# Kernel tuning notes

Measured on AMD Instinct MI355X. Metric: run time of the kernel, lower is better.

## Reference

```python
import jax, jax.numpy as jnp
import numpy as np

N = 50000      # nodes
E = 800000     # edges (avg degree 16)
F_IN = 64      # node_features (== GENConv out, so no input projection)
H = 64         # hidden
EXP = 2 * H    # GENConv MLP expansion dim = 128
D2 = F_IN + H  # dense-block concat dim = SAGEConv in = 128
EPS_MSG = 1e-7 # GENConv message eps
BN_EPS = 1e-5


def setup_inputs() -> dict:
    key = jax.random.key(0)
    ks = jax.random.split(key, 16)
    g = lambda k, shape, fan: jax.random.normal(k, shape, jnp.float32) / np.sqrt(fan)
    return {
        "x": jax.random.normal(ks[0], (N, F_IN), jnp.float32),
        "edge_index": jax.random.randint(ks[1], (2, E), 0, N, jnp.int32),
        # GENConv MLP: Linear(64,128) -> BatchNorm(128) -> ReLU -> Linear(128,64)
        "W1": g(ks[2], (H, EXP), H), "b1": jnp.zeros((EXP,), jnp.float32),
        "gamma": jnp.ones((EXP,), jnp.float32), "beta": jnp.zeros((EXP,), jnp.float32),
        "W2": g(ks[3], (EXP, H), EXP), "b2": jnp.zeros((H,), jnp.float32),
        # SAGEConv project Linear(128,128), lin_l Linear(128,64), lin_r Linear(128,64,bias=False)
        "Wp": g(ks[4], (D2, D2), D2), "bp": jnp.zeros((D2,), jnp.float32),
        "Wl": g(ks[5], (D2, H), D2), "bl": jnp.zeros((H,), jnp.float32),
        "Wr": g(ks[6], (D2, H), D2),
        # fc Linear(64,1)
        "Wf": g(ks[7], (H, 1), H), "bf": jnp.zeros((1,), jnp.float32),
    }


def _forward(x, W1, b1, gamma, beta, W2, b2, Wp, bp, Wl, bl, Wr, Wf, bf, src, dst):
    n = x.shape[0]
    # ---- GENConv(aggr='softmax', t=1.0): msg = relu(x_j) + eps -------------
    msg = jax.nn.relu(x[src]) + EPS_MSG                       # [E, H]
    mmax = jax.ops.segment_max(msg, dst, num_segments=n)      # per-dst, per-feature max
    mmax = jax.lax.stop_gradient(jnp.where(jnp.isfinite(mmax), mmax, 0.0))
    e = jnp.exp(msg - mmax[dst])                              # t = 1.0
    denom = jax.ops.segment_sum(e, dst, num_segments=n)
    numer = jax.ops.segment_sum(e * msg, dst, num_segments=n)
    agg = numer / jnp.where(denom > 0, denom, 1.0)            # softmax aggregation
    out = agg + x                                             # residual with x_dst
    # GENConv MLP (BatchNorm in training mode: batch stats, biased var)
    h = out @ W1 + b1
    mu = h.mean(axis=0)
    var = h.var(axis=0)
    h = (h - mu) * jax.lax.rsqrt(var + BN_EPS) * gamma + beta
    h = jax.nn.relu(h) @ W2 + b2                              # [N, H]
    # ---- DeepGCNLayer block='dense': concat input ---------------------------
    x2 = jnp.concatenate([x, h], axis=-1)                     # [N, F_IN+H]
    x2 = jax.nn.sigmoid(x2)                                   # self.relu = Sigmoid()
    # ---- SAGEConv(project=True, aggr=DeepSetsAggregation()==sum) -----------
    xp = jax.nn.relu(x2 @ Wp + bp)                            # projected source feats
    aggr = jax.ops.segment_sum(xp[src], dst, num_segments=n)  # DeepSets w/o nns = sum
    out2 = aggr @ Wl + bl + x2 @ Wr                           # root uses UNprojected x2
    out2 = jax.nn.sigmoid(out2)
    logits = out2 @ Wf + bf                                   # [N, 1]
    probs = jax.nn.sigmoid(logits)                            # training branch
    return probs, logits


def reference(x, edge_index, W1, b1, gamma, beta, W2, b2, Wp, bp, Wl, bl, Wr, Wf, bf):
    src, dst = edge_index[0], edge_index[1]
    return _forward(x, W1, b1, gamma, beta, W2, b2, Wp, bp, Wl, bl, Wr, Wf, bf, src, dst)
```

## Files before the change

kernel.cpp:

```cpp
#include <hip/hip_runtime.h>

#define F_IN 64
#define HID 64
#define EXPD 128
#define D2 128
#define MAXDEG 64
#define NB 782
#define NBINB 98
#define SUBCAP 40
#define EPT 32

typedef __attribute__((ext_vector_type(8))) short bf16x8;
typedef __attribute__((ext_vector_type(4))) float f32x4;

__device__ __forceinline__ float sigmoidf_(float x) {
    return 1.0f / (1.0f + __expf(-x));
}
__device__ __forceinline__ unsigned bf16rne_(float f) {
    unsigned u = __float_as_uint(f);
    return (u + 0x7FFFu + ((u >> 16) & 1u)) >> 16;
}
__device__ __forceinline__ float bf16tof_(unsigned u16) {
    return __uint_as_float(u16 << 16);
}

__global__ __launch_bounds__(256) void k_bin(const int* __restrict__ ei,
                                             int* __restrict__ cnt2,
                                             unsigned* __restrict__ binned2,
                                             const float* __restrict__ x,
                                             unsigned short* __restrict__ x16,
                                             const float* __restrict__ W1,
                                             const float* __restrict__ W2,
                                             const float* __restrict__ Wp,
                                             const float* __restrict__ Wl,
                                             const float* __restrict__ Wr,
                                             short* __restrict__ dst,
                                             float* __restrict__ bnsums,
                                             int nE, int n, int nbinb) {
    int b = blockIdx.x;
    int tid = threadIdx.x;
    if (b < nbinb) {
        __shared__ int hist[NB];
        if (b == 0) bnsums[tid] = 0.f;
        for (int i = tid; i < NB; i += 256) hist[i] = 0;
        __syncthreads();
        unsigned ed[EPT];
        unsigned short rk[EPT];
        int e0 = b * (256 * EPT);
#pragma unroll
        for (int j = 0; j < EPT; ++j) {
            int e = e0 + j * 256 + tid;
            if (e < nE) {
                unsigned s = (unsigned)ei[e];
                unsigned d = (unsigned)ei[nE + e];
                ed[j] = s | (d << 16);
                rk[j] = (unsigned short)atomicAdd(&hist[d >> 6], 1);
            }
        }
        __syncthreads();
        for (int i = tid; i < NB; i += 256) cnt2[b * NB + i] = hist[i];
#pragma unroll
        for (int j = 0; j < EPT; ++j) {
            int e = e0 + j * 256 + tid;
            if (e < nE) {
                int bin = (ed[j] >> 16) >> 6;
                int r = (int)rk[j];
                if (r < SUBCAP)
                    binned2[((size_t)bin * nbinb + b) * SUBCAP + r] = ed[j];
            }
        }
        return;
    }
    b -= nbinb;
    if (b < 192) {
        int e = b * 256 + tid;
        const float* src;
        int K, N, base2;
        if (e < 8192)       { src = W1; K = 64;  N = 128; base2 = 0; }
        else if (e < 16384) { src = W2; K = 128; N = 64;  base2 = 8192; }
        else if (e < 32768) { src = Wp; K = 128; N = 128; base2 = 16384; }
        else if (e < 40960) { src = Wl; K = 128; N = 64;  base2 = 32768; }
        else                { src = Wr; K = 128; N = 64;  base2 = 40960; }
        int le = e - base2;
        int j = le & 7;
        int lane = (le >> 3) & 63;
        int n16 = lane & 15, q = lane >> 4;
        int rest = le >> 9;
        int KC = K / 32;
        int kc = rest % KC, nt = rest / KC;
        int k = kc * 32 + q * 8 + j;
        int col = nt * 16 + n16;
        dst[e] = (short)bf16rne_(src[(size_t)k * N + col]);
        return;
    }
    int i0 = (b - 192) * 1024 + tid * 4;
    if (i0 < n * F_IN) {
        float4 v = *(const float4*)(x + i0);
        uint2 pk;
        pk.x = bf16rne_(v.x) | (bf16rne_(v.y) << 16);
        pk.y = bf16rne_(v.z) | (bf16rne_(v.w) << 16);
        *(uint2*)(x16 + i0) = pk;
    }
}

__global__ __launch_bounds__(1024) void k_geng(const int* __restrict__ cnt2,
                                               const unsigned* __restrict__ binned2,
                                               const unsigned short* __restrict__ x16,
                                               const short* __restrict__ Wf,
                                               const float* __restrict__ b1,
                                               unsigned short* __restrict__ h16,
                                               float* __restrict__ bnsums,
                                               int* __restrict__ counts,
                                               unsigned short* __restrict__ csr,
                                               int n, int nbinb) {
    __shared__ unsigned short lcsr[64 * MAXDEG];
    __shared__ int lcnt[64];
    __shared__ int scnt[NBINB];
    __shared__ short As[64 * 64];
    __shared__ float bnred[256];
    const unsigned* x32 = (const unsigned*)x16;
    int tid = threadIdx.x;
    int w = tid >> 6;
    int lane = tid & 63;
    int H = lane >> 5, f2 = lane & 31;
    int b = blockIdx.x;
    int rblk = b * 64;
    if (tid < 64) lcnt[tid] = 0;
    if (tid < 256) bnred[tid] = 0.f;
    for (int i = tid; i < nbinb; i += 1024) {
        int c = cnt2[i * NB + b];
        scnt[i] = c < SUBCAP ? c : SUBCAP;
    }
    __syncthreads();
    const unsigned* esrc = binned2 + (size_t)b * nbinb * SUBCAP;
    int tot = nbinb * SUBCAP;
    for (int i = tid; i < tot; i += 1024) {
        int blk = i / SUBCAP;
        int r = i - blk * SUBCAP;
        if (r < scnt[blk]) {
            unsigned u = esrc[i];
            int dl = (int)(u >> 16) - rblk;
            int slot = atomicAdd(&lcnt[dl], 1);
            if (slot < MAXDEG) lcsr[dl * MAXDEG + slot] = (unsigned short)(u & 0xFFFF);
        }
    }
    __syncthreads();
    if (tid < 64 && rblk + tid < n) counts[rblk + tid] = lcnt[tid];
    {
        int nrows = n - rblk;
        nrows = nrows < 64 ? nrows : 64;
        int nu4 = nrows * 8;
        uint4* dstrow = (uint4*)(csr + (size_t)rblk * MAXDEG);
        for (int i = tid; i < nu4; i += 1024) dstrow[i] = ((const uint4*)lcsr)[i];
    }
    for (int t = 0; t < 4; ++t) {
        int rr = w * 4 + t;
        int v = rblk + rr;
        int q8 = f2 >> 2;
        int slot = ((rr >> 4) * 2 + (q8 >> 2)) * 64 + (q8 & 3) * 16 + (rr & 15);
        if (v < n) {
            int deg = lcnt[rr];
            deg = deg > MAXDEG ? MAXDEG : deg;
            int idx = 0;
            if (lane < deg) idx = (int)lcsr[rr * MAXDEG + lane];
            float d0 = 0.f, d1 = 0.f, n0 = 0.f, n1 = 0.f;
            int i = 0;
            for (; i + 16 <= deg; i += 16) {
                unsigned us[8];
#pragma unroll
                for (int tt = 0; tt < 8; ++tt) {
                    int s = __shfl(idx, i + tt * 2 + H, 64);
                    us[tt] = x32[(size_t)s * 32 + f2];
                }
#pragma unroll
                for (int tt = 0; tt < 8; ++tt) {
                    unsigned u = us[tt];
                    float m0 = fmaxf(bf16tof_(u & 0xFFFF), 0.f) + 1e-7f;
                    float m1 = fmaxf(bf16tof_(u >> 16), 0.f) + 1e-7f;
                    float e0 = __expf(m0), e1 = __expf(m1);
                    d0 += e0; d1 += e1;
                    n0 = fmaf(e0, m0, n0);
                    n1 = fmaf(e1, m1, n1);
                }
            }
            for (; i + 8 <= deg; i += 8) {
                int sA = __shfl(idx, i + 0 + H, 64);
                int sB = __shfl(idx, i + 2 + H, 64);
                int sC = __shfl(idx, i + 4 + H, 64);
                int sD = __shfl(idx, i + 6 + H, 64);
                unsigned uA = x32[(size_t)sA * 32 + f2];
                unsigned uB = x32[(size_t)sB * 32 + f2];
                unsigned uC = x32[(size_t)sC * 32 + f2];
                unsigned uD = x32[(size_t)sD * 32 + f2];
#pragma unroll
                for (int tt = 0; tt < 4; ++tt) {
                    unsigned u = tt == 0 ? uA : tt == 1 ? uB : tt == 2 ? uC : uD;
                    float m0 = fmaxf(bf16tof_(u & 0xFFFF), 0.f) + 1e-7f;
                    float m1 = fmaxf(bf16tof_(u >> 16), 0.f) + 1e-7f;
                    float e0 = __expf(m0), e1 = __expf(m1);
                    d0 += e0; d1 += e1;
                    n0 = fmaf(e0, m0, n0);
                    n1 = fmaf(e1, m1, n1);
                }
            }
            for (; i + 2 <= deg; i += 2) {
                int s = __shfl(idx, i + H, 64);
                unsigned u = x32[(size_t)s * 32 + f2];
                float m0 = fmaxf(bf16tof_(u & 0xFFFF), 0.f) + 1e-7f;
                float m1 = fmaxf(bf16tof_(u >> 16), 0.f) + 1e-7f;
                float e0 = __expf(m0), e1 = __expf(m1);
                d0 += e0; d1 += e1;
                n0 = fmaf(e0, m0, n0);
                n1 = fmaf(e1, m1, n1);
            }
            if (i < deg) {
                int s = __shfl(idx, i, 64);
                if (H == 0) {
                    unsigned u = x32[(size_t)s * 32 + f2];
                    float m0 = fmaxf(bf16tof_(u & 0xFFFF), 0.f) + 1e-7f;
                    float m1 = fmaxf(bf16tof_(u >> 16), 0.f) + 1e-7f;
                    float e0 = __expf(m0), e1 = __expf(m1);
                    d0 += e0; d1 += e1;
                    n0 = fmaf(e0, m0, n0);
                    n1 = fmaf(e1, m1, n1);
                }
            }
            d0 += __shfl_xor(d0, 32, 64);
            d1 += __shfl_xor(d1, 32, 64);
            n0 += __shfl_xor(n0, 32, 64);
            n1 += __shfl_xor(n1, 32, 64);
            if (H == 0) {
                float a0 = (deg > 0) ? (n0 / d0) : 0.f;
                float a1 = (deg > 0) ? (n1 / d1) : 0.f;
                unsigned xv = x32[(size_t)v * 32 + f2];
                float r0 = a0 + bf16tof_(xv & 0xFFFF);
                float r1 = a1 + bf16tof_(xv >> 16);
                *(unsigned*)(As + slot * 8 + (f2 & 3) * 2) =
                    bf16rne_(r0) | (bf16rne_(r1) << 16);
            }
        } else {
            if (H == 0) *(unsigned*)(As + slot * 8 + (f2 & 3) * 2) = 0u;
        }
    }
    __syncthreads();
    int L = lane;
    int q = L >> 4, n16 = L & 15;
    int mt = w & 3;
    int nt_base = (w >> 2) * 2;
    f32x4 acc[2];
#pragma unroll
    for (int nt = 0; nt < 2; ++nt) acc[nt] = (f32x4){0.f, 0.f, 0.f, 0.f};
#pragma unroll
    for (int kc = 0; kc < 2; ++kc) {
        bf16x8 a = *(const bf16x8*)(As + ((mt * 2 + kc) * 64 + L) * 8);
#pragma unroll
        for (int nt = 0; nt < 2; ++nt) {
            bf16x8 b2 = *(const bf16x8*)(Wf + (size_t)(((nt_base + nt) * 2 + kc) * 64 + L) * 8);
            acc[nt] = __builtin_amdgcn_mfma_f32_16x16x32_bf16(a, b2, acc[nt], 0, 0, 0);
        }
    }
#pragma unroll
    for (int nt = 0; nt < 2; ++nt) {
        int col = (nt_base + nt) * 16 + n16;
        float bv = b1[col];
        float s = 0.f, s2 = 0.f;
#pragma unroll
        for (int r = 0; r < 4; ++r) {
            int row = rblk + mt * 16 + q * 4 + r;
            float hv = acc[nt][r] + bv;
            if (row < n) {
                h16[(size_t)row * EXPD + col] = (unsigned short)bf16rne_(hv);
                s += hv;
                s2 = fmaf(hv, hv, s2);
            }
        }
        s += __shfl_xor(s, 16, 64);
        s += __shfl_xor(s, 32, 64);
        s2 += __shfl_xor(s2, 16, 64);
        s2 += __shfl_xor(s2, 32, 64);
        if (q == 0) {
            atomicAdd(&bnred[col], s);
            atomicAdd(&bnred[128 + col], s2);
        }
    }
    __syncthreads();
    if (tid < 256) atomicAdd(&bnsums[tid], bnred[tid]);
}

__global__ __launch_bounds__(256) void k_mlp2ab(const unsigned short* __restrict__ h16,
                                                const float* __restrict__ bnsums,
                                                const float* __restrict__ gamma,
                                                const float* __restrict__ beta,
                                                const short* __restrict__ Wf2,
                                                const float* __restrict__ b2,
                                                const unsigned short* __restrict__ x16,
                                                const short* __restrict__ Wfp,
                                                const short* __restrict__ Wfl,
                                                const short* __restrict__ Wfr,
                                                const float* __restrict__ bp,
                                                unsigned short* __restrict__ yp16,
                                                unsigned short* __restrict__ yr16,
                                                float inv_n, int n) {
    __shared__ short Bs[64 * 128];
    __shared__ short As[64 * 128];
    __shared__ float ssl[256];
    int tid = threadIdx.x;
    int rblk = blockIdx.x * 64;
    if (tid < 128) {
        float mu = bnsums[tid] * inv_n;
        float var = fmaf(-mu, mu, bnsums[128 + tid] * inv_n);
        float rs = rsqrtf(fmaxf(var, 0.f) + 1e-5f);
        float scale = gamma[tid] * rs;
        ssl[tid] = scale;
        ssl[128 + tid] = fmaf(-mu, scale, beta[tid]);
    }
    __syncthreads();
#pragma unroll
    for (int it = 0; it < 4; ++it) {
        int c = it * 256 + tid;
        int rr = c & 63, q8 = c >> 6;
        int gr = rblk + rr;
        gr = gr < n ? gr : n - 1;
        uint4 v = *(const uint4*)(h16 + (size_t)gr * EXPD + q8 * 8);
        float4 sc1 = *(const float4*)(ssl + q8 * 8);
        float4 sc2 = *(const float4*)(ssl + q8 * 8 + 4);
        float4 sh1 = *(const float4*)(ssl + 128 + q8 * 8);
        float4 sh2 = *(const float4*)(ssl + 128 + q8 * 8 + 4);
        float o0 = fmaxf(fmaf(bf16tof_(v.x & 0xFFFF), sc1.x, sh1.x), 0.f);
        float o1 = fmaxf(fmaf(bf16tof_(v.x >> 16),    sc1.y, sh1.y), 0.f);
        float o2 = fmaxf(fmaf(bf16tof_(v.y & 0xFFFF), sc1.z, sh1.z), 0.f);
        float o3 = fmaxf(fmaf(bf16tof_(v.y >> 16),    sc1.w, sh1.w), 0.f);
        float o4 = fmaxf(fmaf(bf16tof_(v.z & 0xFFFF), sc2.x, sh2.x), 0.f);
        float o5 = fmaxf(fmaf(bf16tof_(v.z >> 16),    sc2.y, sh2.y), 0.f);
        float o6 = fmaxf(fmaf(bf16tof_(v.w & 0xFFFF), sc2.z, sh2.z), 0.f);
        float o7 = fmaxf(fmaf(bf16tof_(v.w >> 16),    sc2.w, sh2.w), 0.f);
        uint4 pk;
        pk.x = bf16rne_(o0) | (bf16rne_(o1) << 16);
        pk.y = bf16rne_(o2) | (bf16rne_(o3) << 16);
        pk.z = bf16rne_(o4) | (bf16rne_(o5) << 16);
        pk.w = bf16rne_(o6) | (bf16rne_(o7) << 16);
        int slot = ((rr >> 4) * 4 + (q8 >> 2)) * 64 + (q8 & 3) * 16 + (rr & 15);
        *(uint4*)(Bs + slot * 8) = pk;
    }
#pragma unroll
    for (int it = 0; it < 2; ++it) {
        int c = it * 256 + tid;
        int rr = c & 63, q8 = c >> 6;
        int gr = rblk + rr;
        gr = gr < n ? gr : n - 1;
        uint4 v = *(const uint4*)(x16 + (size_t)gr * F_IN + q8 * 8);
        float o0 = sigmoidf_(bf16tof_(v.x & 0xFFFF));
        float o1 = sigmoidf_(bf16tof_(v.x >> 16));
        float o2 = sigmoidf_(bf16tof_(v.y & 0xFFFF));
        float o3 = sigmoidf_(bf16tof_(v.y >> 16));
        float o4 = sigmoidf_(bf16tof_(v.z & 0xFFFF));
        float o5 = sigmoidf_(bf16tof_(v.z >> 16));
        float o6 = sigmoidf_(bf16tof_(v.w & 0xFFFF));
        float o7 = sigmoidf_(bf16tof_(v.w >> 16));
        uint4 pk;
        pk.x = bf16rne_(o0) | (bf16rne_(o1) << 16);
        pk.y = bf16rne_(o2) | (bf16rne_(o3) << 16);
        pk.z = bf16rne_(o4) | (bf16rne_(o5) << 16);
        pk.w = bf16rne_(o6) | (bf16rne_(o7) << 16);
        int slot = ((rr >> 4) * 4 + (q8 >> 2)) * 64 + (q8 & 3) * 16 + (rr & 15);
        *(uint4*)(As + slot * 8) = pk;
    }
    __syncthreads();
    int L = tid & 63, w = tid >> 6;
    int q = L >> 4, n16 = L & 15;
    {
        int mtb = (w & 1) * 2, ntb = (w >> 1) * 2;
        f32x4 acch[2][2];
#pragma unroll
        for (int mt = 0; mt < 2; ++mt)
#pragma unroll
            for (int nt = 0; nt < 2; ++nt) acch[mt][nt] = (f32x4){0.f, 0.f, 0.f, 0.f};
#pragma unroll
        for (int kc = 0; kc < 4; ++kc) {
            bf16x8 a0 = *(const bf16x8*)(Bs + (((mtb + 0) * 4 + kc) * 64 + L) * 8);
            bf16x8 a1 = *(const bf16x8*)(Bs + (((mtb + 1) * 4 + kc) * 64 + L) * 8);
#pragma unroll
            for (int nt = 0; nt < 2; ++nt) {
                bf16x8 b = *(const bf16x8*)(Wf2 + (size_t)(((ntb + nt) * 4 + kc) * 64 + L) * 8);
                acch[0][nt] = __builtin_amdgcn_mfma_f32_16x16x32_bf16(a0, b, acch[0][nt], 0, 0, 0);
                acch[1][nt] = __builtin_amdgcn_mfma_f32_16x16x32_bf16(a1, b, acch[1][nt], 0, 0, 0);
            }
        }
#pragma unroll
        for (int nt = 0; nt < 2; ++nt) {
            int col = (ntb + nt) * 16 + n16;
            float bv = b2[col];
            int q8b = 8 + (col >> 3), jb = col & 7;
#pragma unroll
            for (int mt = 0; mt < 2; ++mt)
#pragma unroll
                for (int r = 0; r < 4; ++r) {
                    int rr2 = (w & 1) * 32 + mt * 16 + q * 4 + r;
                    float hv = sigmoidf_(acch[mt][nt][r] + bv);
                    int slot = ((rr2 >> 4) * 4 + (q8b >> 2)) * 64 + (q8b & 3) * 16 + (rr2 & 15);
                    As[slot * 8 + jb] = (short)bf16rne_(hv);
                }
        }
    }
    __syncthreads();
    int mt_base = (w & 1) * 2;
    int nt_base = (w >> 1) * 4;
    f32x4 acc[2][4];
    f32x4 accr[2][2];
#pragma unroll
    for (int mt = 0; mt < 2; ++mt) {
#pragma unroll
        for (int nt = 0; nt < 4; ++nt) acc[mt][nt] = (f32x4){0.f, 0.f, 0.f, 0.f};
#pragma unroll
        for (int nt = 0; nt < 2; ++nt) accr[mt][nt] = (f32x4){0.f, 0.f, 0.f, 0.f};
    }
#pragma unroll
    for (int kc = 0; kc < 4; ++kc) {
        bf16x8 a0 = *(const bf16x8*)(As + (((mt_base + 0) * 4 + kc) * 64 + L) * 8);
        bf16x8 a1 = *(const bf16x8*)(As + (((mt_base + 1) * 4 + kc) * 64 + L) * 8);
#pragma unroll
        for (int nt = 0; nt < 4; ++nt) {
            bf16x8 b = *(const bf16x8*)(Wfp + (size_t)(((nt_base + nt) * 4 + kc) * 64 + L) * 8);
            acc[0][nt] = __builtin_amdgcn_mfma_f32_16x16x32_bf16(a0, b, acc[0][nt], 0, 0, 0);
            acc[1][nt] = __builtin_amdgcn_mfma_f32_16x16x32_bf16(a1, b, acc[1][nt], 0, 0, 0);
        }
#pragma unroll
        for (int nt = 0; nt < 2; ++nt) {
            bf16x8 b = *(const bf16x8*)(Wfr + (size_t)((((w >> 1) * 2 + nt) * 4 + kc) * 64 + L) * 8);
            accr[0][nt] = __builtin_amdgcn_mfma_f32_16x16x32_bf16(a0, b, accr[0][nt], 0, 0, 0);
            accr[1][nt] = __builtin_amdgcn_mfma_f32_16x16x32_bf16(a1, b, accr[1][nt], 0, 0, 0);
        }
    }
#pragma unroll
    for (int nt = 0; nt < 2; ++nt) {
        int col = ((w >> 1) * 2 + nt) * 16 + n16;
#pragma unroll
        for (int mt = 0; mt < 2; ++mt)
#pragma unroll
            for (int r = 0; r < 4; ++r) {
                int row = rblk + (w & 1) * 32 + mt * 16 + q * 4 + r;
                if (row < n)
                    yr16[(size_t)row * HID + col] = (unsigned short)bf16rne_(accr[mt][nt][r]);
            }
    }
#pragma unroll
    for (int nt = 0; nt < 4; ++nt) {
        int kk = (nt_base + nt) * 16 + n16;
        float bv = bp[kk];
        int q8b = kk >> 3, jb = kk & 7;
#pragma unroll
        for (int mt = 0; mt < 2; ++mt)
#pragma unroll
            for (int r = 0; r < 4; ++r) {
                int rr2 = (w & 1) * 32 + mt * 16 + q * 4 + r;
                float xv = fmaxf(acc[mt][nt][r] + bv, 0.f);
                int slot = ((rr2 >> 4) * 4 + (q8b >> 2)) * 64 + (q8b & 3) * 16 + (rr2 & 15);
                Bs[slot * 8 + jb] = (short)bf16rne_(xv);
            }
    }
    __syncthreads();
    f32x4 acc2[4];
#pragma unroll
    for (int nt = 0; nt < 4; ++nt) acc2[nt] = (f32x4){0.f, 0.f, 0.f, 0.f};
#pragma unroll
    for (int kc = 0; kc < 4; ++kc) {
        bf16x8 a = *(const bf16x8*)(Bs + ((w * 4 + kc) * 64 + L) * 8);
#pragma unroll
        for (int nt = 0; nt < 4; ++nt) {
            bf16x8 b = *(const bf16x8*)(Wfl + (size_t)((nt * 4 + kc) * 64 + L) * 8);
            acc2[nt] = __builtin_amdgcn_mfma_f32_16x16x32_bf16(a, b, acc2[nt], 0, 0, 0);
        }
    }
#pragma unroll
    for (int nt = 0; nt < 4; ++nt) {
        int col = nt * 16 + n16;
#pragma unroll
        for (int r = 0; r < 4; ++r) {
            int row = rblk + w * 16 + q * 4 + r;
            if (row < n)
                yp16[(size_t)row * HID + col] = (unsigned short)bf16rne_(acc2[nt][r]);
        }
    }
}

__global__ __launch_bounds__(256) void k_sagef(const unsigned short* __restrict__ yp16,
                                               const int* __restrict__ counts,
                                               const unsigned short* __restrict__ csr,
                                               const unsigned short* __restrict__ yr16,
                                               const float* __restrict__ bl,
                                               const float* __restrict__ Wfv,
                                               const float* __restrict__ bf,
                                               float* __restrict__ out, int n) {
    const unsigned* yp32 = (const unsigned*)yp16;
    int wid = threadIdx.x >> 6;
    int lane = threadIdx.x & 63;
    int H = lane >> 5, f2 = lane & 31;
    int v = blockIdx.x * 4 + wid;
    if (v >= n) return;
    int deg = counts[v];
    deg = deg > MAXDEG ? MAXDEG : deg;
    int idx = 0;
    if (lane < deg) idx = (int)csr[(size_t)v * MAXDEG + lane];
    float a0 = 0.f, a1 = 0.f;
    int i = 0;
    for (; i + 16 <= deg; i += 16) {
        unsigned us[8];
#pragma unroll
        for (int tt = 0; tt < 8; ++tt) {
            int s = __shfl(idx, i + tt * 2 + H, 64);
            us[tt] = yp32[(size_t)s * 32 + f2];
        }
#pragma unroll
        for (int tt = 0; tt < 8; ++tt) {
            a0 += bf16tof_(us[tt] & 0xFFFF);
            a1 += bf16tof_(us[tt] >> 16);
        }
    }
    for (; i + 8 <= deg; i += 8) {
        int sA = __shfl(idx, i + 0 + H, 64);
        int sB = __shfl(idx, i + 2 + H, 64);
        int sC = __shfl(idx, i + 4 + H, 64);
        int sD = __shfl(idx, i + 6 + H, 64);
        unsigned uA = yp32[(size_t)sA * 32 + f2];
        unsigned uB = yp32[(size_t)sB * 32 + f2];
        unsigned uC = yp32[(size_t)sC * 32 + f2];
        unsigned uD = yp32[(size_t)sD * 32 + f2];
        a0 += bf16tof_(uA & 0xFFFF) + bf16tof_(uB & 0xFFFF) +
              bf16tof_(uC & 0xFFFF) + bf16tof_(uD & 0xFFFF);
        a1 += bf16tof_(uA >> 16) + bf16tof_(uB >> 16) +
              bf16tof_(uC >> 16) + bf16tof_(uD >> 16);
    }
    for (; i + 2 <= deg; i += 2) {
        int s = __shfl(idx, i + H, 64);
        unsigned u = yp32[(size_t)s * 32 + f2];
        a0 += bf16tof_(u & 0xFFFF);
        a1 += bf16tof_(u >> 16);
    }
    if (i < deg) {
        int s = __shfl(idx, i, 64);
        if (H == 0) {
            unsigned u = yp32[(size_t)s * 32 + f2];
            a0 += bf16tof_(u & 0xFFFF);
            a1 += bf16tof_(u >> 16);
        }
    }
    a0 += __shfl_xor(a0, 32, 64);
    a1 += __shfl_xor(a1, 32, 64);
    if (H == 0) {
        unsigned u = ((const unsigned*)yr16)[(size_t)v * 32 + f2];
        float2 blv = ((const float2*)bl)[f2];
        float2 wv  = ((const float2*)Wfv)[f2];
        float o0 = sigmoidf_(a0 + blv.x + bf16tof_(u & 0xFFFF));
        float o1 = sigmoidf_(a1 + blv.y + bf16tof_(u >> 16));
        float t = fmaf(o0, wv.x, o1 * wv.y);
        t += __shfl_xor(t, 1, 64);
        t += __shfl_xor(t, 2, 64);
        t += __shfl_xor(t, 4, 64);
        t += __shfl_xor(t, 8, 64);
        t += __shfl_xor(t, 16, 64);
        if (f2 == 0) {
            float lg = t + bf[0];
            out[v] = sigmoidf_(lg);
            out[n + v] = lg;
        }
    }
}

extern "C" void kernel_launch(void* const* d_in, const int* in_sizes, int n_in,
                              void* d_out, int out_size, void* d_ws, size_t ws_size,
                              hipStream_t stream) {
    const float* x     = (const float*)d_in[0];
    const int*   ei    = (const int*)d_in[1];
    const float* W1    = (const float*)d_in[2];
    const float* b1    = (const float*)d_in[3];
    const float* gamma = (const float*)d_in[4];
    const float* beta  = (const float*)d_in[5];
    const float* W2    = (const float*)d_in[6];
    const float* b2    = (const float*)d_in[7];
    const float* Wp    = (const float*)d_in[8];
    const float* bp    = (const float*)d_in[9];
    const float* Wl    = (const float*)d_in[10];
    const float* bl    = (const float*)d_in[11];
    const float* Wr    = (const float*)d_in[12];
    const float* Wfv   = (const float*)d_in[13];
    const float* bf    = (const float*)d_in[14];
    const int n = in_sizes[0] / F_IN;
    const int e = in_sizes[1] / 2;

    char* ws = (char*)d_ws;
    size_t off = 0;
    auto alloc = [&](size_t bytes) -> void* {
        void* p = (void*)(ws + off);
        off += (bytes + 255) & ~(size_t)255;
        return p;
    };
    const int nbinb = (e + 256 * EPT - 1) / (256 * EPT);
    float*          bnsums   = (float*)alloc(256 * 4);
    int*            cnt2     = (int*)alloc((size_t)nbinb * NB * 4);
    int*            counts   = (int*)alloc((size_t)n * 4);
    unsigned short* csr      = (unsigned short*)alloc((size_t)n * MAXDEG * 2);
    unsigned*       binned2  = (unsigned*)alloc((size_t)NB * nbinb * SUBCAP * 4);
    unsigned short* x16      = (unsigned short*)alloc((size_t)n * F_IN * 2);
    unsigned short* h16      = (unsigned short*)alloc((size_t)n * EXPD * 2);
    unsigned short* yp16     = (unsigned short*)alloc((size_t)n * HID * 2);
    unsigned short* yr16     = (unsigned short*)alloc((size_t)n * HID * 2);
    short*          wfrag    = (short*)alloc(49152 * 2);

    float* out = (float*)d_out;
    const int nb64  = (n + 63) / 64;
    const int nb4   = (n + 3) / 4;
    const int nfp = nbinb + 192 + ((n * F_IN + 1023) / 1024);

    k_bin<<<nfp, 256, 0, stream>>>(ei, cnt2, binned2, x, x16, W1, W2, Wp, Wl,
                                   Wr, wfrag, bnsums, e, n, nbinb);
    k_geng<<<nb64, 1024, 0, stream>>>(cnt2, binned2, x16, wfrag, b1, h16, bnsums,
                                      counts, csr, n, nbinb);
    k_mlp2ab<<<nb64, 256, 0, stream>>>(h16, bnsums, gamma, beta, wfrag + 8192, b2,
                                       x16, wfrag + 16384, wfrag + 32768,
                                       wfrag + 40960, bp, yp16, yr16,
                                       1.0f / (float)n, n);
    k_sagef<<<nb4, 256, 0, stream>>>(yp16, counts, csr, yr16, bl, Wfv, bf, out, n);
}
```

Baseline: 199.9 us.

## Rebuild CSR in shared memory inside SAGE kernel instead of storing it globally

Removes the global CSR and degree-count writes from the GENConv kernel. The final SAGE aggregation kernel now rebuilds each 64-node block's adjacency in shared memory from the binned edge lists, then gathers as before with four rows per wave. This avoids writing and re-reading a large padded CSR buffer. The cost is redoing the binning pass with shared atomics and using larger 1024-thread blocks, which may reduce latency hiding.

```diff
diff --git a/kernel.cpp b/kernel.cpp
--- a/kernel.cpp
+++ b/kernel.cpp
@@ -110,8 +110,6 @@
                                                const float* __restrict__ b1,
                                                unsigned short* __restrict__ h16,
                                                float* __restrict__ bnsums,
-                                               int* __restrict__ counts,
-                                               unsigned short* __restrict__ csr,
                                                int n, int nbinb) {
     __shared__ unsigned short lcsr[64 * MAXDEG];
     __shared__ int lcnt[64];
@@ -145,14 +143,6 @@
         }
     }
     __syncthreads();
-    if (tid < 64 && rblk + tid < n) counts[rblk + tid] = lcnt[tid];
-    {
-        int nrows = n - rblk;
-        nrows = nrows < 64 ? nrows : 64;
-        int nu4 = nrows * 8;
-        uint4* dstrow = (uint4*)(csr + (size_t)rblk * MAXDEG);
-        for (int i = tid; i < nu4; i += 1024) dstrow[i] = ((const uint4*)lcsr)[i];
-    }
     for (int t = 0; t < 4; ++t) {
         int rr = w * 4 + t;
         int v = rblk + rr;
@@ -483,85 +473,114 @@
     }
 }
 
-__global__ __launch_bounds__(256) void k_sagef(const unsigned short* __restrict__ yp16,
-                                               const int* __restrict__ counts,
-                                               const unsigned short* __restrict__ csr,
-                                               const unsigned short* __restrict__ yr16,
-                                               const float* __restrict__ bl,
-                                               const float* __restrict__ Wfv,
-                                               const float* __restrict__ bf,
-                                               float* __restrict__ out, int n) {
+__global__ __launch_bounds__(1024) void k_sagef(const int* __restrict__ cnt2,
+                                                const unsigned* __restrict__ binned2,
+                                                const unsigned short* __restrict__ yp16,
+                                                const unsigned short* __restrict__ yr16,
+                                                const float* __restrict__ bl,
+                                                const float* __restrict__ Wfv,
+                                                const float* __restrict__ bf,
+                                                float* __restrict__ out,
+                                                int n, int nbinb) {
+    __shared__ unsigned short lcsr[64 * MAXDEG];
+    __shared__ int lcnt[64];
+    __shared__ int scnt[NBINB];
     const unsigned* yp32 = (const unsigned*)yp16;
-    int wid = threadIdx.x >> 6;
-    int lane = threadIdx.x & 63;
+    int tid = threadIdx.x;
+    int w = tid >> 6;
+    int lane = tid & 63;
     int H = lane >> 5, f2 = lane & 31;
-    int v = blockIdx.x * 4 + wid;
-    if (v >= n) return;
-    int deg = counts[v];
-    deg = deg > MAXDEG ? MAXDEG : deg;
-    int idx = 0;
-    if (lane < deg) idx = (int)csr[(size_t)v * MAXDEG + lane];
-    float a0 = 0.f, a1 = 0.f;
-    int i = 0;
-    for (; i + 16 <= deg; i += 16) {
-        unsigned us[8];
-#pragma unroll
-        for (int tt = 0; tt < 8; ++tt) {
-            int s = __shfl(idx, i + tt * 2 + H, 64);
-            us[tt] = yp32[(size_t)s * 32 + f2];
-        }
-#pragma unroll
-        for (int tt = 0; tt < 8; ++tt) {
-            a0 += bf16tof_(us[tt] & 0xFFFF);
-            a1 += bf16tof_(us[tt] >> 16);
-        }
-    }
-    for (; i + 8 <= deg; i += 8) {
-        int sA = __shfl(idx, i + 0 + H, 64);
-        int sB = __shfl(idx, i + 2 + H, 64);
-        int sC = __shfl(idx, i + 4 + H, 64);
-        int sD = __shfl(idx, i + 6 + H, 64);
-        unsigned uA = yp32[(size_t)sA * 32 + f2];
-        unsigned uB = yp32[(size_t)sB * 32 + f2];
-        unsigned uC = yp32[(size_t)sC * 32 + f2];
-        unsigned uD = yp32[(size_t)sD * 32 + f2];
-        a0 += bf16tof_(uA & 0xFFFF) + bf16tof_(uB & 0xFFFF) +
-              bf16tof_(uC & 0xFFFF) + bf16tof_(uD & 0xFFFF);
-        a1 += bf16tof_(uA >> 16) + bf16tof_(uB >> 16) +
-              bf16tof_(uC >> 16) + bf16tof_(uD >> 16);
-    }
-    for (; i + 2 <= deg; i += 2) {
-        int s = __shfl(idx, i + H, 64);
-        unsigned u = yp32[(size_t)s * 32 + f2];
-        a0 += bf16tof_(u & 0xFFFF);
-        a1 += bf16tof_(u >> 16);
-    }
-    if (i < deg) {
-        int s = __shfl(idx, i, 64);
-        if (H == 0) {
+    int b = blockIdx.x;
+    int rblk = b * 64;
+    if (tid < 64) lcnt[tid] = 0;
+    for (int i = tid; i < nbinb; i += 1024) {
+        int c = cnt2[i * NB + b];
+        scnt[i] = c < SUBCAP ? c : SUBCAP;
+    }
+    __syncthreads();
+    const unsigned* esrc = binned2 + (size_t)b * nbinb * SUBCAP;
+    int tot = nbinb * SUBCAP;
+    for (int i = tid; i < tot; i += 1024) {
+        int blk = i / SUBCAP;
+        int r = i - blk * SUBCAP;
+        if (r < scnt[blk]) {
+            unsigned u = esrc[i];
+            int dl = (int)(u >> 16) - rblk;
+            int slot = atomicAdd(&lcnt[dl], 1);
+            if (slot < MAXDEG) lcsr[dl * MAXDEG + slot] = (unsigned short)(u & 0xFFFF);
+        }
+    }
+    __syncthreads();
+    for (int t = 0; t < 4; ++t) {
+        int rr = w * 4 + t;
+        int v = rblk + rr;
+        if (v >= n) continue;
+        int deg = lcnt[rr];
+        deg = deg > MAXDEG ? MAXDEG : deg;
+        int idx = 0;
+        if (lane < deg) idx = (int)lcsr[rr * MAXDEG + lane];
+        float a0 = 0.f, a1 = 0.f;
+        int i = 0;
+        for (; i + 16 <= deg; i += 16) {
+            unsigned us[8];
+#pragma unroll
+            for (int tt = 0; tt < 8; ++tt) {
+                int s = __shfl(idx, i + tt * 2 + H, 64);
+                us[tt] = yp32[(size_t)s * 32 + f2];
+            }
+#pragma unroll
+            for (int tt = 0; tt < 8; ++tt) {
+                a0 += bf16tof_(us[tt] & 0xFFFF);
+                a1 += bf16tof_(us[tt] >> 16);
+            }
+        }
+        for (; i + 8 <= deg; i += 8) {
+            int sA = __shfl(idx, i + 0 + H, 64);
+            int sB = __shfl(idx, i + 2 + H, 64);
+            int sC = __shfl(idx, i + 4 + H, 64);
+            int sD = __shfl(idx, i + 6 + H, 64);
+            unsigned uA = yp32[(size_t)sA * 32 + f2];
+            unsigned uB = yp32[(size_t)sB * 32 + f2];
+            unsigned uC = yp32[(size_t)sC * 32 + f2];
+            unsigned uD = yp32[(size_t)sD * 32 + f2];
+            a0 += bf16tof_(uA & 0xFFFF) + bf16tof_(uB & 0xFFFF) +
+                  bf16tof_(uC & 0xFFFF) + bf16tof_(uD & 0xFFFF);
+            a1 += bf16tof_(uA >> 16) + bf16tof_(uB >> 16) +
+                  bf16tof_(uC >> 16) + bf16tof_(uD >> 16);
+        }
+        for (; i + 2 <= deg; i += 2) {
+            int s = __shfl(idx, i + H, 64);
             unsigned u = yp32[(size_t)s * 32 + f2];
             a0 += bf16tof_(u & 0xFFFF);
             a1 += bf16tof_(u >> 16);
         }
-    }
-    a0 += __shfl_xor(a0, 32, 64);
-    a1 += __shfl_xor(a1, 32, 64);
-    if (H == 0) {
-        unsigned u = ((const unsigned*)yr16)[(size_t)v * 32 + f2];
-        float2 blv = ((const float2*)bl)[f2];
-        float2 wv  = ((const float2*)Wfv)[f2];
-        float o0 = sigmoidf_(a0 + blv.x + bf16tof_(u & 0xFFFF));
-        float o1 = sigmoidf_(a1 + blv.y + bf16tof_(u >> 16));
-        float t = fmaf(o0, wv.x, o1 * wv.y);
-        t += __shfl_xor(t, 1, 64);
-        t += __shfl_xor(t, 2, 64);
-        t += __shfl_xor(t, 4, 64);
-        t += __shfl_xor(t, 8, 64);
-        t += __shfl_xor(t, 16, 64);
-        if (f2 == 0) {
-            float lg = t + bf[0];
-            out[v] = sigmoidf_(lg);
-            out[n + v] = lg;
+        if (i < deg) {
+            int s = __shfl(idx, i, 64);
+            if (H == 0) {
+                unsigned u = yp32[(size_t)s * 32 + f2];
+                a0 += bf16tof_(u & 0xFFFF);
+                a1 += bf16tof_(u >> 16);
+            }
+        }
+        a0 += __shfl_xor(a0, 32, 64);
+        a1 += __shfl_xor(a1, 32, 64);
+        if (H == 0) {
+            unsigned u = ((const unsigned*)yr16)[(size_t)v * 32 + f2];
+            float2 blv = ((const float2*)bl)[f2];
+            float2 wv  = ((const float2*)Wfv)[f2];
+            float o0 = sigmoidf_(a0 + blv.x + bf16tof_(u & 0xFFFF));
+            float o1 = sigmoidf_(a1 + blv.y + bf16tof_(u >> 16));
+            float s = fmaf(o0, wv.x, o1 * wv.y);
+            s += __shfl_xor(s, 1, 64);
+            s += __shfl_xor(s, 2, 64);
+            s += __shfl_xor(s, 4, 64);
+            s += __shfl_xor(s, 8, 64);
+            s += __shfl_xor(s, 16, 64);
+            if (f2 == 0) {
+                float lg = s + bf[0];
+                out[v] = sigmoidf_(lg);
+                out[n + v] = lg;
+            }
         }
     }
 }
@@ -597,8 +616,6 @@
     const int nbinb = (e + 256 * EPT - 1) / (256 * EPT);
     float*          bnsums   = (float*)alloc(256 * 4);
     int*            cnt2     = (int*)alloc((size_t)nbinb * NB * 4);
-    int*            counts   = (int*)alloc((size_t)n * 4);
-    unsigned short* csr      = (unsigned short*)alloc((size_t)n * MAXDEG * 2);
     unsigned*       binned2  = (unsigned*)alloc((size_t)NB * nbinb * SUBCAP * 4);
     unsigned short* x16      = (unsigned short*)alloc((size_t)n * F_IN * 2);
     unsigned short* h16      = (unsigned short*)alloc((size_t)n * EXPD * 2);
@@ -608,16 +625,16 @@
 
     float* out = (float*)d_out;
     const int nb64  = (n + 63) / 64;
-    const int nb4   = (n + 3) / 4;
     const int nfp = nbinb + 192 + ((n * F_IN + 1023) / 1024);
 
     k_bin<<<nfp, 256, 0, stream>>>(ei, cnt2, binned2, x, x16, W1, W2, Wp, Wl,
                                    Wr, wfrag, bnsums, e, n, nbinb);
     k_geng<<<nb64, 1024, 0, stream>>>(cnt2, binned2, x16, wfrag, b1, h16, bnsums,
-                                      counts, csr, n, nbinb);
+                                      n, nbinb);
     k_mlp2ab<<<nb64, 256, 0, stream>>>(h16, bnsums, gamma, beta, wfrag + 8192, b2,
                                        x16, wfrag + 16384, wfrag + 32768,
                                        wfrag + 40960, bp, yp16, yr16,
                                        1.0f / (float)n, n);
-    k_sagef<<<nb4, 256, 0, stream>>>(yp16, counts, csr, yr16, bl, Wfv, bf, out, n);
-}
+    k_sagef<<<nb64, 1024, 0, stream>>>(cnt2, binned2, yp16, yr16, bl, Wfv, bf,
+                                       out, n, nbinb);
+}
```

Result: no change. 203.2 us (+1.7%).
